# Kernel optimization log

Measured on AMD Instinct MI355X. Metric: run time of the kernel, lower is better.

## Reference

```python
import jax, jax.numpy as jnp
import numpy as np
from math import factorial as _ft

LMAX = 5
TAU = 32
BATCH = 32
TAUS = [TAU] * (LMAX + 1)
# all (l, l1, l2) satisfying the Clebsch-Gordan triangle condition |l1-l2| <= l <= l1+l2,
# iterated with output degree l as the slow index (matches CGNet's sorted sparse iteration)
LTUPLES = [(l, l1, l2)
           for l in range(LMAX + 1)
           for l1 in range(LMAX + 1)
           for l2 in range(LMAX + 1)
           if abs(l1 - l2) <= l <= l1 + l2]


def _cg_coef(j1, m1, j2, m2, j3, m3):
    """Condon-Shortley Clebsch-Gordan coefficient <j1 m1 j2 m2 | j3 m3> (Racah formula)."""
    if m1 + m2 != m3 or not (abs(j1 - j2) <= j3 <= j1 + j2):
        return 0.0
    pref = np.sqrt((2 * j3 + 1) * _ft(j3 + j1 - j2) * _ft(j3 - j1 + j2)
                   * _ft(j1 + j2 - j3) / _ft(j1 + j2 + j3 + 1))
    pref *= np.sqrt(_ft(j3 + m3) * _ft(j3 - m3) * _ft(j1 - m1) * _ft(j1 + m1)
                    * _ft(j2 - m2) * _ft(j2 + m2))
    s = 0.0
    for k in range(j1 + j2 - j3 + 1):
        args = (k, j1 + j2 - j3 - k, j1 - m1 - k, j2 + m2 - k,
                j3 - j2 + m1 + k, j3 - j1 - m2 + k)
        if min(args) < 0:
            continue
        den = 1.0
        for a in args:
            den *= _ft(a)
        s += (-1.0) ** k / den
    return pref * s


def _cg_mat(l1, l2, l):
    """CG block of shape [2l+1, (2l1+1)*(2l2+1)], column index (m1+l1)*(2l2+1)+(m2+l2)."""
    M = np.zeros((2 * l + 1, (2 * l1 + 1) * (2 * l2 + 1)), dtype=np.float64)
    for m in range(-l, l + 1):
        for m1 in range(-l1, l1 + 1):
            m2 = m - m1
            if abs(m2) <= l2:
                M[m + l, (m1 + l1) * (2 * l2 + 1) + (m2 + l2)] = _cg_coef(l1, m1, l2, m2, l, m)
    return jnp.asarray(M, dtype=jnp.float32)


CG_MATS = {(l1, l2, l): _cg_mat(l1, l2, l) for (l, l1, l2) in LTUPLES}
TOTAL_IN = sum(TAUS[l] * (2 * l + 1) * 2 for l in range(LMAX + 1))  # 2304


def setup_inputs() -> dict:
    key = jax.random.key(0)
    fs = jax.random.normal(key, (BATCH, TOTAL_IN), dtype=jnp.float32)
    return {"fs": fs}


def reference(fs):
    B = fs.shape[0]
    # split flat input into per-l fragments [B, 2l+1, tau_l, (re,im)]
    parts, off = [], 0
    for l in range(LMAX + 1):
        n = TAUS[l] * (2 * l + 1) * 2
        p = fs[:, off:off + n].reshape(B, TAUS[l], 2 * l + 1, 2)
        parts.append(jnp.transpose(p, (0, 2, 1, 3)))
        off += n

    def kron(x, y):
        # batched Kronecker product over the last two axes:
        # [B,m1,t1] x [B,m2,t2] -> [B, m1*m2, t1*t2]
        m1, t1 = x.shape[1:3]
        m2, t2 = y.shape[1:3]
        return jnp.einsum('bit,bju->bijtu', x, y).reshape(B, m1 * m2, t1 * t2)

    outs = [[] for _ in range(LMAX + 1)]
    for (l, l1, l2) in LTUPLES:
        a, b = parts[l1], parts[l2]
        ar, ai = a[..., 0], a[..., 1]
        br, bi = b[..., 0], b[..., 1]
        # complex Kronecker product
        kr = kron(ar, br) - kron(ai, bi)
        ki = kron(ar, bi) + kron(ai, br)
        # CG contraction (real CG matrix applied to both components)
        C = CG_MATS[(l1, l2, l)]  # [2l+1, (2l1+1)(2l2+1)]
        FFl = jnp.stack([jnp.einsum('mk,bkt->bmt', C, kr),
                         jnp.einsum('mk,bkt->bmt', C, ki)], axis=-1)
        outs[l].append(jnp.transpose(FFl, (0, 2, 1, 3)))  # [B, tau1*tau2, 2l+1, 2]

    new_fs = [jnp.concatenate(o, axis=1) for o in outs]
    # straight_output=True branch: flatten per-l blocks and concatenate
    return jnp.concatenate([f.reshape(B, -1, 2) for f in new_fs], axis=1)
```

## Files before the change

### kernel.cpp

```cpp
#include <hip/hip_runtime.h>

#define NT     111
#define LMAX   5
#define TAU    32
#define NBATCH 32
#define ROW    2304

struct Tup { int l, l1, l2, out_off, in1, in2; };
struct Meta { Tup t[NT]; int totch; };

constexpr int IN_OFF[LMAX + 1] = {0, 64, 256, 576, 1024, 1600};

constexpr Meta make_meta() {
  Meta m{};
  int n = 0, out = 0;
  for (int l = 0; l <= LMAX; ++l)
    for (int l1 = 0; l1 <= LMAX; ++l1)
      for (int l2 = 0; l2 <= LMAX; ++l2) {
        int df = l1 - l2; if (df < 0) df = -df;
        if (df <= l && l <= l1 + l2) {
          m.t[n].l = l; m.t[n].l1 = l1; m.t[n].l2 = l2;
          m.t[n].out_off = out;
          m.t[n].in1 = IN_OFF[l1]; m.t[n].in2 = IN_OFF[l2];
          out += TAU * TAU * (2 * l + 1);
          ++n;
        }
      }
  m.totch = out;
  return m;
}

constexpr Meta META  = make_meta();
constexpr int  TOTCH = META.totch;

constexpr double cfact(int n) { double r = 1.0; for (int i = 2; i <= n; ++i) r *= i; return r; }

constexpr double csqrt(double x) {
  if (x <= 0.0) return 0.0;
  double g = x;
  for (int i = 0; i < 100; ++i) g = 0.5 * (g + x / g);
  return g;
}

constexpr double cg_coef_ct(int j1, int m1, int j2, int m2, int j3, int m3) {
  if (m1 + m2 != m3) return 0.0;
  double pref = csqrt((2.0 * j3 + 1.0) * cfact(j3 + j1 - j2) * cfact(j3 - j1 + j2) *
                      cfact(j1 + j2 - j3) / cfact(j1 + j2 + j3 + 1));
  pref *= csqrt(cfact(j3 + m3) * cfact(j3 - m3) * cfact(j1 - m1) * cfact(j1 + m1) *
                cfact(j2 - m2) * cfact(j2 + m2));
  double s = 0.0;
  const int kmax = j1 + j2 - j3;
  for (int k = 0; k <= kmax; ++k) {
    const int a3 = j1 - m1 - k, a4 = j2 + m2 - k, a5 = j3 - j2 + m1 + k, a6 = j3 - j1 - m2 + k;
    if (a3 < 0 || a4 < 0 || a5 < 0 || a6 < 0) continue;
    const double den = cfact(k) * cfact(kmax - k) * cfact(a3) * cfact(a4) * cfact(a5) * cfact(a6);
    s += ((k & 1) ? -1.0 : 1.0) / den;
  }
  return pref * s;
}

template<int L, int L1, int L2>
struct CGTab {
  struct T { float v[2 * L + 1][2 * L1 + 1][2 * L2 + 1]; };
  static constexpr T gen() {
    T t{};
    for (int m = 0; m < 2 * L + 1; ++m)
      for (int i1 = 0; i1 < 2 * L1 + 1; ++i1)
        for (int i2 = 0; i2 < 2 * L2 + 1; ++i2)
          t.v[m][i1][i2] = (float)cg_coef_ct(L1, i1 - L1, L2, i2 - L2, L, m - L);
    return t;
  }
  static constexpr T tab = gen();
};

template<int L, int L1, int L2>
__device__ __forceinline__ void tuple_impl(const float* __restrict__ fa,
                                           const float* __restrict__ fb,
                                           float2* __restrict__ po) {
  constexpr int D = 2 * L + 1, D1 = 2 * L1 + 1, D2 = 2 * L2 + 1;
  const int tid = threadIdx.x;

  const int t2 = tid & 31;
  float br[D2], bi[D2];
  const float2* pb = (const float2*)fb + t2 * D2;
  #pragma unroll
  for (int i = 0; i < D2; ++i) { float2 v = pb[i]; br[i] = v.x; bi[i] = v.y; }

  #pragma unroll
  for (int j = 0; j < 4; ++j) {
    const int tp = tid + 256 * j;
    const int t1 = tp >> 5;

    float ar[D1], ai[D1];
    const float2* pa = (const float2*)fa + t1 * D1;
    #pragma unroll
    for (int i = 0; i < D1; ++i) { float2 v = pa[i]; ar[i] = v.x; ai[i] = v.y; }

    float2 res[D];
    #pragma unroll
    for (int m = 0; m < D; ++m) {
      float re = 0.f, im = 0.f;
      #pragma unroll
      for (int i1 = 0; i1 < D1; ++i1) {
        const int i2 = (m - L) - (i1 - L1) + L2;
        if (i2 >= 0 && i2 < D2) {
          const float c = CGTab<L, L1, L2>::tab.v[m][i1][i2];
          if (c != 0.f) {
            re += c * (ar[i1] * br[i2] - ai[i1] * bi[i2]);
            im += c * (ar[i1] * bi[i2] + ai[i1] * br[i2]);
          }
        }
      }
      res[m] = make_float2(re, im);
    }

    float2* o = po + tp * D;
    #pragma unroll
    for (int m = 0; m < D; ++m) o[m] = res[m];
  }
}

template<int I>
__device__ __forceinline__ void dispatch(int idx, int b,
                                         const float* __restrict__ fs,
                                         float2* __restrict__ out) {
  if constexpr (I < NT) {
    if (idx == I) {
      constexpr Tup t = META.t[I];
      tuple_impl<t.l, t.l1, t.l2>(fs + b * ROW + t.in1,
                                  fs + b * ROW + t.in2,
                                  out + (size_t)b * TOTCH + t.out_off);
    } else {
      dispatch<I + 1>(idx, b, fs, out);
    }
  }
}

__global__ void __launch_bounds__(256)
cg_main(const float* __restrict__ fs, float2* __restrict__ out) {
  dispatch<0>(blockIdx.x, blockIdx.y, fs, out);
}

extern "C" void kernel_launch(void* const* d_in, const int* in_sizes, int n_in,
                              void* d_out, int out_size, void* d_ws, size_t ws_size,
                              hipStream_t stream) {
  const float* fs = (const float*)d_in[0];
  float2* out = (float2*)d_out;
  (void)d_ws; (void)ws_size; (void)in_sizes; (void)n_in; (void)out_size;

  cg_main<<<dim3(NT, NBATCH), dim3(256), 0, stream>>>(fs, out);
}
```

Measured before the change: 241.0 us.

## Replace templated per-tuple dispatch with generic shared-memory staged kernel and coalesced stores

Removes the 111-way compile-time dispatch chain and instead reads per-tuple metadata and a flattened CG table from device memory at runtime. Input fragments and CG coefficients are staged in LDS. Results are written to shared memory first and then stored as coalesced float4 writes, replacing the strided per-thread float2 stores. In exchange the inner loops are no longer fully unrolled with compile-time constants, so there are more index computations, extra LDS traffic and added barriers.

Result: faster. 218.2 us (-9.4%).

```diff
diff --git a/kernel.cpp b/kernel.cpp
--- a/kernel.cpp
+++ b/kernel.cpp
@@ -1,4 +1,6 @@
 #include <hip/hip_runtime.h>
+#include <utility>
+#include <cstddef>
 
 #define NT     111
 #define LMAX   5
@@ -6,32 +8,32 @@
 #define NBATCH 32
 #define ROW    2304
 
-struct Tup { int l, l1, l2, out_off, in1, in2; };
-struct Meta { Tup t[NT]; int totch; };
+struct Tup { int l, l1, l2, out_off, in1, in2, cg_off; };
+struct Meta { Tup t[NT]; int totch, totcg; };
 
 constexpr int IN_OFF[LMAX + 1] = {0, 64, 256, 576, 1024, 1600};
 
 constexpr Meta make_meta() {
   Meta m{};
-  int n = 0, out = 0;
+  int n = 0, out = 0, cg = 0;
   for (int l = 0; l <= LMAX; ++l)
     for (int l1 = 0; l1 <= LMAX; ++l1)
       for (int l2 = 0; l2 <= LMAX; ++l2) {
         int df = l1 - l2; if (df < 0) df = -df;
         if (df <= l && l <= l1 + l2) {
-          m.t[n].l = l; m.t[n].l1 = l1; m.t[n].l2 = l2;
-          m.t[n].out_off = out;
-          m.t[n].in1 = IN_OFF[l1]; m.t[n].in2 = IN_OFF[l2];
+          m.t[n] = Tup{l, l1, l2, out, IN_OFF[l1], IN_OFF[l2], cg};
           out += TAU * TAU * (2 * l + 1);
+          cg  += (2 * l + 1) * (2 * l1 + 1);
           ++n;
         }
       }
-  m.totch = out;
+  m.totch = out; m.totcg = cg;
   return m;
 }
 
 constexpr Meta META  = make_meta();
 constexpr int  TOTCH = META.totch;
+constexpr int  TOTCG = META.totcg;
 
 constexpr double cfact(int n) { double r = 1.0; for (int i = 2; i <= n; ++i) r *= i; return r; }
 
@@ -59,86 +61,101 @@
   return pref * s;
 }
 
-template<int L, int L1, int L2>
-struct CGTab {
-  struct T { float v[2 * L + 1][2 * L1 + 1][2 * L2 + 1]; };
+template<int I>
+struct CGC {
+  static constexpr int L  = META.t[I].l, L1 = META.t[I].l1, L2 = META.t[I].l2;
+  static constexpr int D = 2 * L + 1, D1 = 2 * L1 + 1, D2 = 2 * L2 + 1;
+  struct T { float v[D * D1]; };
   static constexpr T gen() {
     T t{};
-    for (int m = 0; m < 2 * L + 1; ++m)
-      for (int i1 = 0; i1 < 2 * L1 + 1; ++i1)
-        for (int i2 = 0; i2 < 2 * L2 + 1; ++i2)
-          t.v[m][i1][i2] = (float)cg_coef_ct(L1, i1 - L1, L2, i2 - L2, L, m - L);
+    for (int m = 0; m < D; ++m)
+      for (int i1 = 0; i1 < D1; ++i1) {
+        const int i2 = (m - L) - (i1 - L1) + L2;
+        t.v[m * D1 + i1] = (i2 >= 0 && i2 < D2)
+            ? (float)cg_coef_ct(L1, i1 - L1, L2, i2 - L2, L, m - L) : 0.0f;
+      }
     return t;
   }
   static constexpr T tab = gen();
 };
 
-template<int L, int L1, int L2>
-__device__ __forceinline__ void tuple_impl(const float* __restrict__ fa,
-                                           const float* __restrict__ fb,
-                                           float2* __restrict__ po) {
-  constexpr int D = 2 * L + 1, D1 = 2 * L1 + 1, D2 = 2 * L2 + 1;
-  const int tid = threadIdx.x;
-
-  const int t2 = tid & 31;
-  float br[D2], bi[D2];
-  const float2* pb = (const float2*)fb + t2 * D2;
-  #pragma unroll
-  for (int i = 0; i < D2; ++i) { float2 v = pb[i]; br[i] = v.x; bi[i] = v.y; }
-
-  #pragma unroll
-  for (int j = 0; j < 4; ++j) {
-    const int tp = tid + 256 * j;
-    const int t1 = tp >> 5;
-
-    float ar[D1], ai[D1];
-    const float2* pa = (const float2*)fa + t1 * D1;
-    #pragma unroll
-    for (int i = 0; i < D1; ++i) { float2 v = pa[i]; ar[i] = v.x; ai[i] = v.y; }
-
-    float2 res[D];
-    #pragma unroll
-    for (int m = 0; m < D; ++m) {
-      float re = 0.f, im = 0.f;
-      #pragma unroll
-      for (int i1 = 0; i1 < D1; ++i1) {
-        const int i2 = (m - L) - (i1 - L1) + L2;
-        if (i2 >= 0 && i2 < D2) {
-          const float c = CGTab<L, L1, L2>::tab.v[m][i1][i2];
-          if (c != 0.f) {
-            re += c * (ar[i1] * br[i2] - ai[i1] * bi[i2]);
-            im += c * (ar[i1] * bi[i2] + ai[i1] * br[i2]);
-          }
-        }
-      }
-      res[m] = make_float2(re, im);
-    }
-
-    float2* o = po + tp * D;
-    #pragma unroll
-    for (int m = 0; m < D; ++m) o[m] = res[m];
-  }
-}
+struct Flat { float v[TOTCG]; };
 
 template<int I>
-__device__ __forceinline__ void dispatch(int idx, int b,
-                                         const float* __restrict__ fs,
-                                         float2* __restrict__ out) {
-  if constexpr (I < NT) {
-    if (idx == I) {
-      constexpr Tup t = META.t[I];
-      tuple_impl<t.l, t.l1, t.l2>(fs + b * ROW + t.in1,
-                                  fs + b * ROW + t.in2,
-                                  out + (size_t)b * TOTCH + t.out_off);
-    } else {
-      dispatch<I + 1>(idx, b, fs, out);
-    }
-  }
+constexpr void copy_one(Flat& f) {
+  constexpr int n = (2 * META.t[I].l + 1) * (2 * META.t[I].l1 + 1);
+  for (int k = 0; k < n; ++k) f.v[META.t[I].cg_off + k] = CGC<I>::tab.v[k];
 }
+template<std::size_t... Is>
+constexpr Flat build_flat(std::index_sequence<Is...>) {
+  Flat f{};
+  (copy_one<(int)Is>(f), ...);
+  return f;
+}
+constexpr Flat CG_FLAT_H = build_flat(std::make_index_sequence<NT>{});
+
+__device__ const Flat CG_FLAT = CG_FLAT_H;
+__device__ const Meta D_META  = META;
 
 __global__ void __launch_bounds__(256)
 cg_main(const float* __restrict__ fs, float2* __restrict__ out) {
-  dispatch<0>(blockIdx.x, blockIdx.y, fs, out);
+  __shared__ float  s_re[256 * 11];
+  __shared__ float  s_im[256 * 11];
+  __shared__ float2 s_b[32 * 11];
+  __shared__ float2 s_a[8 * 11];
+  __shared__ float  s_cg[121];
+
+  const int tid = threadIdx.x;
+  const Tup tp  = D_META.t[blockIdx.x];
+  const int L = tp.l, L1 = tp.l1, L2 = tp.l2;
+  const int D = 2 * L + 1, D1 = 2 * L1 + 1, D2 = 2 * L2 + 1;
+  const int b = blockIdx.y;
+
+  const float2* fa = (const float2*)(fs + b * ROW + tp.in1);
+  const float2* fb = (const float2*)(fs + b * ROW + tp.in2);
+  float2* po = out + (size_t)b * TOTCH + tp.out_off;
+
+  for (int i = tid; i < D * D1; i += 256) s_cg[i] = CG_FLAT.v[tp.cg_off + i];
+  {
+    const int r = tid & 31;
+    for (int c = tid >> 5; c < D2; c += 8) s_b[r * D2 + c] = fb[r * D2 + c];
+  }
+
+  const int t1l  = tid >> 5;
+  const int t2   = tid & 31;
+  const int resb = tid * D;
+
+  for (int j = 0; j < 4; ++j) {
+    if ((tid >> 3) < D1)
+      s_a[(tid & 7) * D1 + (tid >> 3)] = fa[(8 * j + (tid & 7)) * D1 + (tid >> 3)];
+    __syncthreads();
+
+    const float2* pa = s_a + t1l * D1;
+    const float2* pb = s_b + t2 * D2;
+    const float*  cgrow = s_cg;
+    for (int m = 0; m < D; ++m, cgrow += D1) {
+      const int S = m - L + L1 + L2;
+      int lo = S - (D2 - 1); if (lo < 0) lo = 0;
+      int hi = S;            if (hi > D1 - 1) hi = D1 - 1;
+      float re = 0.f, im = 0.f;
+      for (int i1 = lo; i1 <= hi; ++i1) {
+        const float  c  = cgrow[i1];
+        const float2 a  = pa[i1];
+        const float2 bb = pb[S - i1];
+        re += c * (a.x * bb.x - a.y * bb.y);
+        im += c * (a.x * bb.y + a.y * bb.x);
+      }
+      s_re[resb + m] = re;
+      s_im[resb + m] = im;
+    }
+    __syncthreads();
+
+    float4* oj4 = (float4*)(po + (size_t)(256 * j) * D);
+    const int NV = 128 * D;
+    for (int e = tid; e < NV; e += 256)
+      oj4[e] = make_float4(s_re[2 * e], s_im[2 * e],
+                           s_re[2 * e + 1], s_im[2 * e + 1]);
+  }
 }
 
 extern "C" void kernel_launch(void* const* d_in, const int* in_sizes, int n_in,
```

## Stage per-wave outputs in LDS for coalesced float4 global stores

Applied to the files above, without the earlier changes.

Each wave writes its D-wide complex results into a per-wave shared-memory staging buffer, then copies the buffer to global memory as contiguous float4 stores, replacing strided per-thread float2 writes. The tuple dispatch becomes a binary search instead of a linear if-chain, and the j loop is no longer unrolled, which should reduce code size and register pressure. The kernel now uses a shared staging buffer and relies on manual s_waitcnt barriers that are only valid within a wave, so correctness depends on wave-synchronous execution.

Result: faster. 198.7 us (-17.6%).

```diff
diff --git a/kernel.cpp b/kernel.cpp
--- a/kernel.cpp
+++ b/kernel.cpp
@@ -76,9 +76,13 @@
 template<int L, int L1, int L2>
 __device__ __forceinline__ void tuple_impl(const float* __restrict__ fa,
                                            const float* __restrict__ fb,
-                                           float2* __restrict__ po) {
+                                           float2* __restrict__ po,
+                                           float2* __restrict__ stage) {
   constexpr int D = 2 * L + 1, D1 = 2 * L1 + 1, D2 = 2 * L2 + 1;
-  const int tid = threadIdx.x;
+  const int tid  = threadIdx.x;
+  const int lane = tid & 63;
+  const int wv   = tid >> 6;
+  float2* swave = stage + wv * (64 * D);
 
   const int t2 = tid & 31;
   float br[D2], bi[D2];
@@ -86,7 +90,7 @@
   #pragma unroll
   for (int i = 0; i < D2; ++i) { float2 v = pb[i]; br[i] = v.x; bi[i] = v.y; }
 
-  #pragma unroll
+  #pragma unroll 1
   for (int j = 0; j < 4; ++j) {
     const int tp = tid + 256 * j;
     const int t1 = tp >> 5;
@@ -114,31 +118,48 @@
       res[m] = make_float2(re, im);
     }
 
-    float2* o = po + tp * D;
-    #pragma unroll
-    for (int m = 0; m < D; ++m) o[m] = res[m];
+    if constexpr (D == 1) {
+      po[tp] = res[0];
+    } else {
+      asm volatile("s_waitcnt lgkmcnt(0)" ::: "memory");
+      #pragma unroll
+      for (int m = 0; m < D; ++m) swave[lane * D + m] = res[m];
+      asm volatile("s_waitcnt lgkmcnt(0)" ::: "memory");
+
+      const float4* s4  = (const float4*)swave;
+      float4*       ow4 = (float4*)(po + (size_t)(256 * j + 64 * wv) * D);
+      #pragma unroll
+      for (int k = 0; k <= (D - 1) / 2; ++k) {
+        const int f = lane + 64 * k;
+        if (k < (D - 1) / 2 || lane < 32)
+          ow4[f] = s4[f];
+      }
+    }
   }
 }
 
-template<int I>
+template<int LO, int HI>
 __device__ __forceinline__ void dispatch(int idx, int b,
                                          const float* __restrict__ fs,
-                                         float2* __restrict__ out) {
-  if constexpr (I < NT) {
-    if (idx == I) {
-      constexpr Tup t = META.t[I];
-      tuple_impl<t.l, t.l1, t.l2>(fs + b * ROW + t.in1,
-                                  fs + b * ROW + t.in2,
-                                  out + (size_t)b * TOTCH + t.out_off);
-    } else {
-      dispatch<I + 1>(idx, b, fs, out);
-    }
+                                         float2* __restrict__ out,
+                                         float2* __restrict__ stage) {
+  if constexpr (HI - LO == 1) {
+    constexpr Tup t = META.t[LO];
+    tuple_impl<t.l, t.l1, t.l2>(fs + b * ROW + t.in1,
+                                fs + b * ROW + t.in2,
+                                out + (size_t)b * TOTCH + t.out_off,
+                                stage);
+  } else {
+    constexpr int MID = LO + (HI - LO) / 2;
+    if (idx < MID) dispatch<LO, MID>(idx, b, fs, out, stage);
+    else           dispatch<MID, HI>(idx, b, fs, out, stage);
   }
 }
 
 __global__ void __launch_bounds__(256)
 cg_main(const float* __restrict__ fs, float2* __restrict__ out) {
-  dispatch<0>(blockIdx.x, blockIdx.y, fs, out);
+  __shared__ float2 stage[4 * 64 * 11];
+  dispatch<0, NT>(blockIdx.x, blockIdx.y, fs, out, stage);
 }
 
 extern "C" void kernel_launch(void* const* d_in, const int* in_sizes, int n_in,
```
